# Kernel tuning notes

Hardware: AMD Instinct MI355X
Metric: run time of the kernel (lower is better)

## Reference

```python
import jax, jax.numpy as jnp
import numpy as np

EPS = 1e-5

def _ln(x, g, b):
    m = jnp.mean(x, axis=-1, keepdims=True)
    v = jnp.var(x, axis=-1, keepdims=True)
    return (x - m) / jnp.sqrt(v + EPS) * g + b

def _lin(x, w, b):
    # torch-style weight [out, in]
    return x @ w.T + b

def _mlp(x, w1, b1, w2, b2):
    # Mlp: Linear -> exact GELU -> Linear (dropout=0)
    return _lin(jax.nn.gelu(_lin(x, w1, b1), approximate=False), w2, b2)

def setup_inputs() -> dict:
    B, C, H, W = 2, 256, 64, 64
    key = jax.random.key(0)
    ks = jax.random.split(key, 32)
    s = 0.02  # param init scale keeps attention logits in a sane range
    d = {
        'center_fea': jax.random.normal(ks[0], (B, C, H, W), jnp.float32),
        'wh_fea':     jax.random.normal(ks[1], (B, C, H, W), jnp.float32),
        'cls_fea':    jax.random.normal(ks[2], (B, C, H, W), jnp.float32),
        'mix_w': jax.random.normal(ks[3], (C, 3 * C), jnp.float32) * s,
        'mix_b': jnp.zeros((C,), jnp.float32),
        'ln_g': jnp.ones((C,), jnp.float32),
        'ln_b': jnp.zeros((C,), jnp.float32),
        'q1_w': jax.random.normal(ks[4], (C, C), jnp.float32) * s,
        'q1_b': jnp.zeros((C,), jnp.float32),
        'q2_w': jax.random.normal(ks[5], (C, C), jnp.float32) * s,
        'q2_b': jnp.zeros((C,), jnp.float32),
        'q3_w': jax.random.normal(ks[6], (C, C), jnp.float32) * s,
        'q3_b': jnp.zeros((C,), jnp.float32),
        'k_w': jax.random.normal(ks[7], (C, C), jnp.float32) * s,
        'k_b': jnp.zeros((C,), jnp.float32),
        'v_w': jax.random.normal(ks[8], (C, C), jnp.float32) * s,
        'v_b': jnp.zeros((C,), jnp.float32),
        'cmlp_w1': jax.random.normal(ks[9], (C, C), jnp.float32) * s,
        'cmlp_b1': jnp.zeros((C,), jnp.float32),
        'cmlp_w2': jax.random.normal(ks[10], (C, C), jnp.float32) * s,
        'cmlp_b2': jnp.zeros((C,), jnp.float32),
        'wmlp_w1': jax.random.normal(ks[11], (C, C), jnp.float32) * s,
        'wmlp_b1': jnp.zeros((C,), jnp.float32),
        'wmlp_w2': jax.random.normal(ks[12], (C, C), jnp.float32) * s,
        'wmlp_b2': jnp.zeros((C,), jnp.float32),
        'clsmlp_w1': jax.random.normal(ks[13], (C, C), jnp.float32) * s,
        'clsmlp_b1': jnp.zeros((C,), jnp.float32),
        'clsmlp_w2': jax.random.normal(ks[14], (C, C), jnp.float32) * s,
        'clsmlp_b2': jnp.zeros((C,), jnp.float32),
    }
    return d

def reference(center_fea, wh_fea, cls_fea, mix_w, mix_b, ln_g, ln_b,
              q1_w, q1_b, q2_w, q2_b, q3_w, q3_b, k_w, k_b, v_w, v_b,
              cmlp_w1, cmlp_b1, cmlp_w2, cmlp_b2,
              wmlp_w1, wmlp_b1, wmlp_w2, wmlp_b2,
              clsmlp_w1, clsmlp_b1, clsmlp_w2, clsmlp_b2):
    b, c, h, w = center_fea.shape
    # 1x1 conv mix over concatenated channels [b, 3c, h, w] -> [b, c, h, w]
    cat = jnp.concatenate([center_fea, wh_fea, cls_fea], axis=1)
    mix = jnp.einsum('oc,bchw->bohw', mix_w, cat) + mix_b[None, :, None, None]

    tok = lambda x: x.reshape(b, c, h * w).transpose(0, 2, 1)  # [b, N, c]
    cf, wf, clf, mf = tok(center_fea), tok(wh_fea), tok(cls_fea), tok(mix)

    ct, wt, clt, mt = _ln(cf, ln_g, ln_b), _ln(wf, ln_g, ln_b), _ln(clf, ln_g, ln_b), _ln(mf, ln_g, ln_b)

    kf = _lin(mt, k_w, k_b)  # shared K
    vf = _lin(mt, v_w, v_b)  # shared V

    def attend(q):
        score = jax.nn.softmax(jnp.einsum('bnd,bmd->bnm', q, kf), axis=-1)  # [b, N, N]
        return jnp.einsum('bnm,bmd->bnd', score, vf)

    cf  = _ln(cf  + attend(_lin(ct,  q1_w, q1_b)), ln_g, ln_b)
    wf  = _ln(wf  + attend(_lin(wt,  q2_w, q2_b)), ln_g, ln_b)
    clf = _ln(clf + attend(_lin(clt, q3_w, q3_b)), ln_g, ln_b)

    cf  = _ln(cf  + _mlp(cf,  cmlp_w1, cmlp_b1, cmlp_w2, cmlp_b2), ln_g, ln_b)
    wf  = _ln(wf  + _mlp(wf,  wmlp_w1, wmlp_b1, wmlp_w2, wmlp_b2), ln_g, ln_b)
    clf = _ln(clf + _mlp(clf, clsmlp_w1, clsmlp_b1, clsmlp_w2, clsmlp_b2), ln_g, ln_b)

    untok = lambda x: x.transpose(0, 2, 1).reshape(b, c, h, w)
    return (untok(cf), untok(wf), untok(clf))
```

## Files before the change

kernel.cpp:

```cpp
#include <hip/hip_runtime.h>
#include <hip/hip_bf16.h>
#include <math.h>

typedef unsigned int   u32;
typedef unsigned short u16;
typedef float floatx4 __attribute__((ext_vector_type(4)));
typedef short bf16x8  __attribute__((ext_vector_type(8)));

#define MFMA16(a,b,c) __builtin_amdgcn_mfma_f32_16x16x32_bf16((a),(b),(c),0,0,0)

static __device__ __forceinline__ float bfbits2f(u16 h){
    return __uint_as_float(((u32)h) << 16);
}
static __device__ __forceinline__ u16 f2bfbits(float f){
    u32 u = __float_as_uint(f);
    u32 r = (u + 0x7fffu + ((u >> 16) & 1u)) >> 16;
    return (u16)r;
}
static __device__ __forceinline__ bool sniff_bf16(const void* ln_g){
    return ((const u32*)ln_g)[0] == 0x3f803f80u;
}

typedef __attribute__((address_space(1))) const unsigned int gas_u32;
typedef __attribute__((address_space(3))) unsigned int las_u32;
static __device__ __forceinline__ void gl_lds16(const void* g, void* l){
    __builtin_amdgcn_global_load_lds((gas_u32*)g, (las_u32*)l, 16, 0, 0);
}

#define DPPF(v, ctrl) __uint_as_float((u32)__builtin_amdgcn_update_dpp( \
        (int)__float_as_uint(v), (int)__float_as_uint(v), (ctrl), 0xf, 0xf, true))

static __device__ __forceinline__ float red16_max(float v){
    v = fmaxf(v, DPPF(v, 0xB1));
    v = fmaxf(v, DPPF(v, 0x4E));
    v = fmaxf(v, DPPF(v, 0x141));
    v = fmaxf(v, DPPF(v, 0x140));
    return v;
}
static __device__ __forceinline__ float red16_sum(float v){
    v += DPPF(v, 0xB1);
    v += DPPF(v, 0x4E);
    v += DPPF(v, 0x141);
    v += DPPF(v, 0x140);
    return v;
}

struct PackJob { const void* src; void* dst; int n; int mode; };
struct PackParams { PackJob jobs[26]; const void* lng; };

__global__ __launch_bounds__(256) void k_pack(PackParams p){
    bool isb = sniff_bf16(p.lng);
    PackJob j = p.jobs[blockIdx.y];
    for (int i = blockIdx.x * 256 + threadIdx.x; i < j.n; i += 256 * 256){
        float v = isb ? bfbits2f(((const u16*)j.src)[i]) : ((const float*)j.src)[i];
        if (j.mode == 0) ((u16*)j.dst)[i]  = f2bfbits(v);
        else             ((float*)j.dst)[i] = v;
    }
}

struct FtParams { const void* src[3]; u16* dst[3]; const void* lng; };

__global__ __launch_bounds__(256) void k_feat_t(FtParams p){
    bool isb = sniff_bf16(p.lng);
    int z = blockIdx.z; int si = z >> 1; int b = z & 1;
    const void* src = p.src[si]; u16* dst = p.dst[si];
    int n0 = blockIdx.x * 64, c0 = blockIdx.y * 64;
    __shared__ float tile[64][65];
    int t = threadIdx.x; int tx = t & 63; int ty = t >> 6;
    #pragma unroll
    for (int pp = 0; pp < 16; ++pp){
        int cl = ty + pp * 4;
        size_t off = ((size_t)b * 256 + c0 + cl) * 4096 + n0 + tx;
        float v = isb ? bfbits2f(((const u16*)src)[off]) : ((const float*)src)[off];
        tile[cl][tx] = v;
    }
    __syncthreads();
    #pragma unroll
    for (int pp = 0; pp < 16; ++pp){
        int nl = ty + pp * 4; int cl = tx;
        dst[((size_t)b * 4096 + n0 + nl) * 256 + c0 + cl] = f2bfbits(tile[cl][nl]);
    }
}

struct GemmJob { const u16* A0; const u16* A1; const u16* A2;
                 const u16* W; const float* bias; const u16* res; u16* out; };
struct GemmParams { GemmJob jobs[5]; int K; int op; };

__global__ __launch_bounds__(256, 3) void k_gemm(GemmParams p){
    GemmJob j = p.jobs[blockIdx.z];
    int m0 = blockIdx.x * 128, n0 = blockIdx.y * 128;
    __shared__ __align__(16) u16 As[128][64];
    __shared__ __align__(16) u16 Bs[128][64];
    int t = threadIdx.x;
    int wave = t >> 6, lane = t & 63, l15 = lane & 15, quad = lane >> 4;
    int mh = (wave & 1) * 64, nh = (wave >> 1) * 64;
    int key = l15 & 7;

    floatx4 acc[4][4];
    #pragma unroll
    for (int a = 0; a < 4; ++a)
        #pragma unroll
        for (int bq = 0; bq < 4; ++bq) acc[a][bq] = (floatx4){0.f,0.f,0.f,0.f};

    for (int k0 = 0; k0 < p.K; k0 += 64){
        __syncthreads();
        const u16* Ap = (k0 < 256) ? j.A0 : (k0 < 512 ? j.A1 : j.A2);
        int koff = k0 & 255;
        #pragma unroll
        for (int m = 0; m < 4; ++m){
            int r  = (wave * 4 + m) * 8 + (lane >> 3);
            int gs = (lane & 7) ^ (r & 7);
            gl_lds16(Ap  + (size_t)(m0 + r) * 256 + koff + gs * 8, &As[(wave*4+m)*8][0]);
            gl_lds16(j.W + (size_t)(n0 + r) * p.K + k0   + gs * 8, &Bs[(wave*4+m)*8][0]);
        }
        __syncthreads();

        #pragma unroll
        for (int kc = 0; kc < 2; ++kc){
            bf16x8 av[4], bv[4];
            #pragma unroll
            for (int mb = 0; mb < 4; ++mb)
                av[mb] = *(const bf16x8*)&As[mh + mb*16 + l15][(((kc*4 + quad) ^ key)) * 8];
            #pragma unroll
            for (int nb = 0; nb < 4; ++nb)
                bv[nb] = *(const bf16x8*)&Bs[nh + nb*16 + l15][(((kc*4 + quad) ^ key)) * 8];
            #pragma unroll
            for (int mb = 0; mb < 4; ++mb)
                #pragma unroll
                for (int nb = 0; nb < 4; ++nb)
                    acc[mb][nb] = MFMA16(av[mb], bv[nb], acc[mb][nb]);
        }
    }

    #pragma unroll
    for (int mb = 0; mb < 4; ++mb)
        #pragma unroll
        for (int nb = 0; nb < 4; ++nb){
            int col = n0 + nh + nb * 16 + l15;
            float bias = j.bias[col];
            #pragma unroll
            for (int rg = 0; rg < 4; ++rg){
                int row = m0 + mh + mb * 16 + quad * 4 + rg;
                float v = acc[mb][nb][rg] + bias;
                if (p.op == 1)      v = 0.5f * v * (1.0f + erff(v * 0.70710678118f));
                else if (p.op == 2) v += bfbits2f(j.res[(size_t)row * 256 + col]);
                j.out[(size_t)row * 256 + col] = f2bfbits(v);
            }
        }
}

struct LnJob { const u16* src; u16* dst; };
struct LnParams { LnJob jobs[4]; const float* g; const float* b; };

__global__ __launch_bounds__(256, 4) void k_ln(LnParams p){
    LnJob j = p.jobs[blockIdx.y];
    int g16 = threadIdx.x >> 4, l = threadIdx.x & 15;
    size_t tok = (size_t)blockIdx.x * 16 + g16;
    const u16* row = j.src + tok * 256 + l * 16;
    uint4 ra = *(const uint4*)(row);
    uint4 rb = *(const uint4*)(row + 8);
    u32 wv[8] = {ra.x, ra.y, ra.z, ra.w, rb.x, rb.y, rb.z, rb.w};
    float va[16];
    float s1 = 0.f, s2 = 0.f;
    #pragma unroll
    for (int i = 0; i < 8; ++i){
        float a = bfbits2f((u16)(wv[i] & 0xffffu));
        float c = bfbits2f((u16)(wv[i] >> 16));
        va[2*i] = a; va[2*i+1] = c;
        s1 += a + c; s2 += a*a + c*c;
    }
    s1 = red16_sum(s1); s2 = red16_sum(s2);
    float mean = s1 * (1.f/256.f);
    float var  = s2 * (1.f/256.f) - mean * mean;
    float rstd = rsqrtf(var + 1e-5f);
    int c0 = l * 16;
    u32 ow[8];
    #pragma unroll
    for (int i = 0; i < 8; ++i){
        float x0 = (va[2*i]   - mean) * rstd * p.g[c0 + 2*i]     + p.b[c0 + 2*i];
        float x1 = (va[2*i+1] - mean) * rstd * p.g[c0 + 2*i + 1] + p.b[c0 + 2*i + 1];
        ow[i] = (u32)f2bfbits(x0) | ((u32)f2bfbits(x1) << 16);
    }
    u16* dst = j.dst + tok * 256 + c0;
    *(uint4*)(dst)     = (uint4){ow[0], ow[1], ow[2], ow[3]};
    *(uint4*)(dst + 8) = (uint4){ow[4], ow[5], ow[6], ow[7]};
}

__global__ __launch_bounds__(256, 4) void k_vt(const u16* __restrict__ Vf, u16* __restrict__ Vt){
    int b = blockIdx.z;
    int n0 = blockIdx.x * 64, c0 = blockIdx.y * 64;
    __shared__ u16 tile[64][66];
    int t = threadIdx.x; int tx = t & 63; int ty = t >> 6;
    #pragma unroll
    for (int pp = 0; pp < 16; ++pp){
        int nl = ty + pp * 4;
        tile[nl][tx] = Vf[((size_t)b * 4096 + n0 + nl) * 256 + c0 + tx];
    }
    __syncthreads();
    #pragma unroll
    for (int pp = 0; pp < 16; ++pp){
        int cl = ty + pp * 4; int nl = tx;
        Vt[((size_t)b * 256 + c0 + cl) * 4096 + n0 + nl] = tile[nl][cl];
    }
}

struct FlashParams {
    const u16* Q[3]; const u16* K; const u16* Vt;
    const u16* Res[3]; u16* Out[3];
    const float* g; const float* b;
};

__global__ __launch_bounds__(256, 2) void k_flash(FlashParams p){
    int s = blockIdx.y >> 1, b = blockIdx.y & 1;
    int m0 = blockIdx.x * 64;
    const u16* Q   = p.Q[s]   + (size_t)b * 4096 * 256;
    const u16* Kf  = p.K      + (size_t)b * 4096 * 256;
    const u16* Vtg = p.Vt     + (size_t)b * 256 * 4096;
    const u16* Res = p.Res[s] + (size_t)b * 4096 * 256;
    u16*       Out = p.Out[s] + (size_t)b * 4096 * 256;

    __shared__ __align__(16) u16 Kb[2][32][256];
    __shared__ __align__(16) u16 Vb[2][256][32];
    __shared__ __align__(16) u16 Pl[4][16][40];

    int t = threadIdx.x, wave = t >> 6, lane = t & 63, l15 = lane & 15, quad = lane >> 4;

    auto stage = [&](int bi, int kv0){
        #pragma unroll
        for (int m = 0; m < 4; ++m){
            int q = wave * 4 + m;
            int r0 = q * 2 + (lane >> 5);
            int gg = (lane & 31) ^ (r0 & 7);
            gl_lds16(Kf + (size_t)(kv0 + r0) * 256 + gg * 8, &Kb[bi][q * 2][0]);
        }
        #pragma unroll
        for (int m = 0; m < 4; ++m){
            int q = wave * 4 + m;
            int d = q * 16 + (lane >> 2);
            int gg = (lane & 3) ^ ((d >> 1) & 3);
            gl_lds16(Vtg + (size_t)d * 4096 + kv0 + gg * 8, &Vb[bi][q * 16][0]);
        }
    };

    stage(0, 0);

    bf16x8 qf[8];
    {
        const u16* qrow = Q + (size_t)(m0 + wave * 16 + l15) * 256 + quad * 8;
        #pragma unroll
        for (int kc = 0; kc < 8; ++kc) qf[kc] = *(const bf16x8*)(qrow + kc * 32);
    }
    floatx4 o[16];
    #pragma unroll
    for (int i = 0; i < 16; ++i) o[i] = (floatx4){0.f,0.f,0.f,0.f};
    float mrow[4] = {-INFINITY,-INFINITY,-INFINITY,-INFINITY};
    float lsum[4] = {0.f,0.f,0.f,0.f};

    __syncthreads();
    int buf = 0;

    for (int ch = 0; ch < 128; ++ch){
        if (ch < 127) stage(buf ^ 1, (ch + 1) * 32);

        floatx4 sa[2];
        #pragma unroll
        for (int sub = 0; sub < 2; ++sub){
            int row = sub * 16 + l15;
            floatx4 a0 = (floatx4){0.f,0.f,0.f,0.f};
            floatx4 a1 = (floatx4){0.f,0.f,0.f,0.f};
            #pragma unroll
            for (int kc = 0; kc < 4; ++kc){
                bf16x8 kb0 = *(const bf16x8*)&Kb[buf][row][((((2*kc  ) * 4 + quad) ^ (row & 7))) * 8];
                bf16x8 kb1 = *(const bf16x8*)&Kb[buf][row][((((2*kc+1) * 4 + quad) ^ (row & 7))) * 8];
                a0 = MFMA16(qf[2*kc  ], kb0, a0);
                a1 = MFMA16(qf[2*kc+1], kb1, a1);
            }
            sa[sub] = a0 + a1;
        }

        float al[4]; int grow = 0;
        #pragma unroll
        for (int rg = 0; rg < 4; ++rg){
            float m1 = red16_max(fmaxf(sa[0][rg], sa[1][rg]));
            grow |= (m1 > mrow[rg]) ? 1 : 0;
            float mn = fmaxf(mrow[rg], m1);
            al[rg] = __expf(mrow[rg] - mn);
            mrow[rg] = mn;
        }
        #pragma unroll
        for (int rg = 0; rg < 4; ++rg){
            float p0 = __expf(sa[0][rg] - mrow[rg]);
            float p1 = __expf(sa[1][rg] - mrow[rg]);
            sa[0][rg] = p0; sa[1][rg] = p1;
            lsum[rg] = lsum[rg] * al[rg] + (p0 + p1);
        }

        #pragma unroll
        for (int sub = 0; sub < 2; ++sub)
            #pragma unroll
            for (int rg = 0; rg < 4; ++rg)
                Pl[wave][quad * 4 + rg][sub * 16 + l15] = f2bfbits(sa[sub][rg]);

        if (__any(grow)){
            #pragma unroll
            for (int dc = 0; dc < 16; ++dc)
                #pragma unroll
                for (int rg = 0; rg < 4; ++rg) o[dc][rg] *= al[rg];
        }

        asm volatile("s_waitcnt lgkmcnt(0)" ::: "memory");
        __builtin_amdgcn_sched_barrier(0);

        bf16x8 pa = *(const bf16x8*)&Pl[wave][l15][quad * 8];
        #pragma unroll
        for (int dc = 0; dc < 16; ++dc){
            int row = dc * 16 + l15;
            bf16x8 vb = *(const bf16x8*)&Vb[buf][row][((quad ^ ((row >> 1) & 3))) * 8];
            o[dc] = MFMA16(pa, vb, o[dc]);
        }

        __syncthreads();
        buf ^= 1;
    }

    float inv[4];
    #pragma unroll
    for (int rg = 0; rg < 4; ++rg) inv[rg] = 1.0f / red16_sum(lsum[rg]);
    float s1[4] = {0.f,0.f,0.f,0.f}, s2[4] = {0.f,0.f,0.f,0.f};
    #pragma unroll
    for (int dc = 0; dc < 16; ++dc)
        #pragma unroll
        for (int rg = 0; rg < 4; ++rg){
            int row = m0 + wave * 16 + quad * 4 + rg;
            float v = o[dc][rg] * inv[rg] + bfbits2f(Res[(size_t)row * 256 + dc * 16 + l15]);
            o[dc][rg] = v;
            s1[rg] += v; s2[rg] += v * v;
        }
    #pragma unroll
    for (int rg = 0; rg < 4; ++rg){
        float mean = red16_sum(s1[rg]) * (1.f/256.f);
        float q2   = red16_sum(s2[rg]);
        float var  = q2 * (1.f/256.f) - mean * mean;
        s1[rg] = mean; s2[rg] = rsqrtf(var + 1e-5f);
    }
    #pragma unroll
    for (int dc = 0; dc < 16; ++dc){
        int c = dc * 16 + l15;
        float gv = p.g[c], bv = p.b[c];
        #pragma unroll
        for (int rg = 0; rg < 4; ++rg){
            int row = m0 + wave * 16 + quad * 4 + rg;
            Out[(size_t)row * 256 + c] = f2bfbits((o[dc][rg] - s1[rg]) * s2[rg] * gv + bv);
        }
    }
}

struct OutTParams { const u16* F[3]; void* out; const void* lng; };

__global__ __launch_bounds__(256, 4) void k_out_t(OutTParams p){
    bool isb = sniff_bf16(p.lng);
    int z = blockIdx.z; int s = z >> 1; int b = z & 1;
    const u16* F = p.F[s];
    int n0 = blockIdx.x * 64, c0 = blockIdx.y * 64;
    __shared__ u16 tile[64][66];
    int t = threadIdx.x; int tx = t & 63; int ty = t >> 6;
    #pragma unroll
    for (int pp = 0; pp < 16; ++pp){
        int nl = ty + pp * 4;
        tile[nl][tx] = F[((size_t)b * 4096 + n0 + nl) * 256 + c0 + tx];
    }
    __syncthreads();
    size_t obase = ((size_t)s * 2 + b) * 256 * 4096;
    #pragma unroll
    for (int pp = 0; pp < 16; ++pp){
        int cl = ty + pp * 4; int nl = tx;
        u16 raw = tile[nl][cl];
        size_t off = obase + (size_t)(c0 + cl) * 4096 + n0 + nl;
        if (isb) ((u16*)p.out)[off]   = raw;
        else     ((float*)p.out)[off] = bfbits2f(raw);
    }
}

extern "C" void kernel_launch(void* const* d_in, const int* in_sizes, int n_in,
                              void* d_out, int out_size, void* d_ws, size_t ws_size,
                              hipStream_t stream) {
    (void)in_sizes; (void)n_in; (void)out_size; (void)ws_size;
    const size_t SLOT = (size_t)2 * 4096 * 256;
    u16* ws = (u16*)d_ws;
    auto slot = [&](int i){ return ws + (size_t)i * SLOT; };

    u16 *Tc = slot(0),  *Tw = slot(1),  *Tcl = slot(2),  *Tm = slot(3);
    u16 *Lc = slot(4),  *Lw = slot(5),  *Lcl = slot(6),  *Lm = slot(7);
    u16 *Q1 = slot(8),  *Q2 = slot(9),  *Q3  = slot(10);
    u16 *Kf = slot(11), *Vf = slot(12), *Vt  = slot(13);
    u16 *Yc = slot(14), *Yw = slot(15), *Ycl = slot(16);
    u16 *Hc = Q1, *Hw = Q2, *Hcl = Q3;
    u16 *Zc = Lc, *Zw = Lw, *Zcl = Lcl;
    u16 *Fc = Kf, *Fw = Vf, *Fcl = Vt;

    u16* wbase = slot(17);
    u16 *mixw = wbase;
    u16 *q1w = wbase + 196608, *q2w = q1w + 65536, *q3w = q2w + 65536;
    u16 *kw  = q3w + 65536,    *vw  = kw  + 65536;
    u16 *cw1 = vw  + 65536, *cw2 = cw1 + 65536, *ww1 = cw2 + 65536,
        *ww2 = ww1 + 65536, *clw1 = ww2 + 65536, *clw2 = clw1 + 65536;
    float* pbase = (float*)(wbase + 1048576);
    float *mixb = pbase,        *lng = pbase+256,  *lnb = pbase+512,
          *q1b = pbase+768,  *q2b = pbase+1024, *q3b = pbase+1280,
          *kb  = pbase+1536, *vb  = pbase+1792,
          *cb1 = pbase+2048, *cb2 = pbase+2304, *wb1 = pbase+2560,
          *wb2 = pbase+2816, *clb1= pbase+3072, *clb2= pbase+3328;

    {
        PackParams pp;
        const int widx[12] = {3,7,9,11,13,15,17,19,21,23,25,27};
        u16* wdst[12] = {mixw,q1w,q2w,q3w,kw,vw,cw1,cw2,ww1,ww2,clw1,clw2};
        for (int i = 0; i < 12; ++i)
            pp.jobs[i] = PackJob{ d_in[widx[i]], wdst[i], (i==0?196608:65536), 0 };
        const int pidx[14] = {4,5,6,8,10,12,14,16,18,20,22,24,26,28};
        float* pdst[14] = {mixb,lng,lnb,q1b,q2b,q3b,kb,vb,cb1,cb2,wb1,wb2,clb1,clb2};
        for (int i = 0; i < 14; ++i)
            pp.jobs[12+i] = PackJob{ d_in[pidx[i]], pdst[i], 256, 1 };
        pp.lng = d_in[5];
        hipLaunchKernelGGL(k_pack, dim3(256, 26), dim3(256), 0, stream, pp);
    }
    {
        FtParams fp;
        fp.src[0] = d_in[0]; fp.src[1] = d_in[1]; fp.src[2] = d_in[2];
        fp.dst[0] = Tc; fp.dst[1] = Tw; fp.dst[2] = Tcl;
        fp.lng = d_in[5];
        hipLaunchKernelGGL(k_feat_t, dim3(64, 4, 6), dim3(256), 0, stream, fp);
    }
    {
        GemmParams gp; gp.K = 768; gp.op = 0;
        gp.jobs[0] = GemmJob{ Tc, Tw, Tcl, mixw, mixb, nullptr, Tm };
        hipLaunchKernelGGL(k_gemm, dim3(64, 2, 1), dim3(256), 0, stream, gp);
    }
    {
        LnParams lp; lp.g = lng; lp.b = lnb;
        lp.jobs[0] = LnJob{Tc, Lc}; lp.jobs[1] = LnJob{Tw, Lw};
        lp.jobs[2] = LnJob{Tcl, Lcl}; lp.jobs[3] = LnJob{Tm, Lm};
        hipLaunchKernelGGL(k_ln, dim3(512, 4), dim3(256), 0, stream, lp);
    }
    {
        GemmParams gp; gp.K = 256; gp.op = 0;
        gp.jobs[0] = GemmJob{ Lc,  nullptr, nullptr, q1w, q1b, nullptr, Q1 };
        gp.jobs[1] = GemmJob{ Lw,  nullptr, nullptr, q2w, q2b, nullptr, Q2 };
        gp.jobs[2] = GemmJob{ Lcl, nullptr, nullptr, q3w, q3b, nullptr, Q3 };
        gp.jobs[3] = GemmJob{ Lm,  nullptr, nullptr, kw,  kb,  nullptr, Kf };
        gp.jobs[4] = GemmJob{ Lm,  nullptr, nullptr, vw,  vb,  nullptr, Vf };
        hipLaunchKernelGGL(k_gemm, dim3(64, 2, 5), dim3(256), 0, stream, gp);
    }
    hipLaunchKernelGGL(k_vt, dim3(64, 4, 2), dim3(256), 0, stream, Vf, Vt);
    {
        FlashParams fp;
        fp.Q[0] = Q1; fp.Q[1] = Q2; fp.Q[2] = Q3;
        fp.K = Kf; fp.Vt = Vt;
        fp.Res[0] = Tc; fp.Res[1] = Tw; fp.Res[2] = Tcl;
        fp.Out[0] = Yc; fp.Out[1] = Yw; fp.Out[2] = Ycl;
        fp.g = lng; fp.b = lnb;
        hipLaunchKernelGGL(k_flash, dim3(64, 6), dim3(256), 0, stream, fp);
    }
    {
        GemmParams gp; gp.K = 256; gp.op = 1;
        gp.jobs[0] = GemmJob{ Yc,  nullptr, nullptr, cw1,  cb1,  nullptr, Hc };
        gp.jobs[1] = GemmJob{ Yw,  nullptr, nullptr, ww1,  wb1,  nullptr, Hw };
        gp.jobs[2] = GemmJob{ Ycl, nullptr, nullptr, clw1, clb1, nullptr, Hcl };
        hipLaunchKernelGGL(k_gemm, dim3(64, 2, 3), dim3(256), 0, stream, gp);
    }
    {
        GemmParams gp; gp.K = 256; gp.op = 2;
        gp.jobs[0] = GemmJob{ Hc,  nullptr, nullptr, cw2,  cb2,  Yc,  Zc };
        gp.jobs[1] = GemmJob{ Hw,  nullptr, nullptr, ww2,  wb2,  Yw,  Zw };
        gp.jobs[2] = GemmJob{ Hcl, nullptr, nullptr, clw2, clb2, Ycl, Zcl };
        hipLaunchKernelGGL(k_gemm, dim3(64, 2, 3), dim3(256), 0, stream, gp);
    }
    {
        LnParams lp; lp.g = lng; lp.b = lnb;
        lp.jobs[0] = LnJob{Zc, Fc}; lp.jobs[1] = LnJob{Zw, Fw};
        lp.jobs[2] = LnJob{Zcl, Fcl}; lp.jobs[3] = LnJob{Zc, Fc};
        hipLaunchKernelGGL(k_ln, dim3(512, 3), dim3(256), 0, stream, lp);
    }
    {
        OutTParams op;
        op.F[0] = Fc; op.F[1] = Fw; op.F[2] = Fcl;
        op.out = d_out; op.lng = d_in[5];
        hipLaunchKernelGGL(k_out_t, dim3(64, 4, 6), dim3(256), 0, stream, op);
    }
}
```

Before: 468.1 us.

## Shrink GEMM tiles to 64x64 with double-buffered LDS and raise flash MFMA priority

The shared GEMM kernel moves from 128x128 to 64x64 output tiles, with double-buffered LDS staging so the next K-slice loads while the current one is computed. The grid grows fourfold so more of the CUs are busy on these small GEMMs. The flash attention kernel wraps its MFMA sections in s_setprio to favor matrix issue across waves. Smaller tiles reduce per-block data reuse and add more global traffic.

```diff
diff --git a/kernel.cpp b/kernel.cpp
--- a/kernel.cpp
+++ b/kernel.cpp
@@ -86,56 +86,61 @@
                  const u16* W; const float* bias; const u16* res; u16* out; };
 struct GemmParams { GemmJob jobs[5]; int K; int op; };
 
-__global__ __launch_bounds__(256, 3) void k_gemm(GemmParams p){
+__global__ __launch_bounds__(256, 4) void k_gemm(GemmParams p){
     GemmJob j = p.jobs[blockIdx.z];
-    int m0 = blockIdx.x * 128, n0 = blockIdx.y * 128;
-    __shared__ __align__(16) u16 As[128][64];
-    __shared__ __align__(16) u16 Bs[128][64];
+    int m0 = blockIdx.x * 64, n0 = blockIdx.y * 64;
+    __shared__ __align__(16) u16 As[2][64][64];
+    __shared__ __align__(16) u16 Bs[2][64][64];
     int t = threadIdx.x;
     int wave = t >> 6, lane = t & 63, l15 = lane & 15, quad = lane >> 4;
-    int mh = (wave & 1) * 64, nh = (wave >> 1) * 64;
+    int mh = (wave & 1) * 32, nh = (wave >> 1) * 32;
     int key = l15 & 7;
 
-    floatx4 acc[4][4];
-    #pragma unroll
-    for (int a = 0; a < 4; ++a)
-        #pragma unroll
-        for (int bq = 0; bq < 4; ++bq) acc[a][bq] = (floatx4){0.f,0.f,0.f,0.f};
-
-    for (int k0 = 0; k0 < p.K; k0 += 64){
-        __syncthreads();
+    auto stage = [&](int bi, int k0){
         const u16* Ap = (k0 < 256) ? j.A0 : (k0 < 512 ? j.A1 : j.A2);
         int koff = k0 & 255;
         #pragma unroll
-        for (int m = 0; m < 4; ++m){
-            int r  = (wave * 4 + m) * 8 + (lane >> 3);
+        for (int i = 0; i < 2; ++i){
+            int rq = wave * 2 + i;
+            int r  = rq * 8 + (lane >> 3);
             int gs = (lane & 7) ^ (r & 7);
-            gl_lds16(Ap  + (size_t)(m0 + r) * 256 + koff + gs * 8, &As[(wave*4+m)*8][0]);
-            gl_lds16(j.W + (size_t)(n0 + r) * p.K + k0   + gs * 8, &Bs[(wave*4+m)*8][0]);
+            gl_lds16(Ap  + (size_t)(m0 + r) * 256 + koff + gs * 8, &As[bi][rq * 8][0]);
+            gl_lds16(j.W + (size_t)(n0 + r) * p.K + k0   + gs * 8, &Bs[bi][rq * 8][0]);
+        }
+    };
+
+    floatx4 acc[2][2];
+    #pragma unroll
+    for (int a = 0; a < 2; ++a)
+        #pragma unroll
+        for (int bq = 0; bq < 2; ++bq) acc[a][bq] = (floatx4){0.f,0.f,0.f,0.f};
+
+    stage(0, 0);
+    __syncthreads();
+    int nk = p.K >> 6, buf = 0;
+
+    for (int ks = 0; ks < nk; ++ks){
+        if (ks + 1 < nk) stage(buf ^ 1, (ks + 1) * 64);
+        #pragma unroll
+        for (int kc = 0; kc < 2; ++kc){
+            int gsel = ((kc * 4 + quad) ^ key) * 8;
+            bf16x8 a0 = *(const bf16x8*)&As[buf][mh +      l15][gsel];
+            bf16x8 a1 = *(const bf16x8*)&As[buf][mh + 16 + l15][gsel];
+            bf16x8 b0 = *(const bf16x8*)&Bs[buf][nh +      l15][gsel];
+            bf16x8 b1 = *(const bf16x8*)&Bs[buf][nh + 16 + l15][gsel];
+            acc[0][0] = MFMA16(a0, b0, acc[0][0]);
+            acc[0][1] = MFMA16(a0, b1, acc[0][1]);
+            acc[1][0] = MFMA16(a1, b0, acc[1][0]);
+            acc[1][1] = MFMA16(a1, b1, acc[1][1]);
         }
         __syncthreads();
-
-        #pragma unroll
-        for (int kc = 0; kc < 2; ++kc){
-            bf16x8 av[4], bv[4];
-            #pragma unroll
-            for (int mb = 0; mb < 4; ++mb)
-                av[mb] = *(const bf16x8*)&As[mh + mb*16 + l15][(((kc*4 + quad) ^ key)) * 8];
-            #pragma unroll
-            for (int nb = 0; nb < 4; ++nb)
-                bv[nb] = *(const bf16x8*)&Bs[nh + nb*16 + l15][(((kc*4 + quad) ^ key)) * 8];
-            #pragma unroll
-            for (int mb = 0; mb < 4; ++mb)
-                #pragma unroll
-                for (int nb = 0; nb < 4; ++nb)
-                    acc[mb][nb] = MFMA16(av[mb], bv[nb], acc[mb][nb]);
-        }
-    }
-
-    #pragma unroll
-    for (int mb = 0; mb < 4; ++mb)
-        #pragma unroll
-        for (int nb = 0; nb < 4; ++nb){
+        buf ^= 1;
+    }
+
+    #pragma unroll
+    for (int mb = 0; mb < 2; ++mb)
+        #pragma unroll
+        for (int nb = 0; nb < 2; ++nb){
             int col = n0 + nh + nb * 16 + l15;
             float bias = j.bias[col];
             #pragma unroll
@@ -263,6 +268,7 @@
         if (ch < 127) stage(buf ^ 1, (ch + 1) * 32);
 
         floatx4 sa[2];
+        __builtin_amdgcn_s_setprio(1);
         #pragma unroll
         for (int sub = 0; sub < 2; ++sub){
             int row = sub * 16 + l15;
@@ -277,6 +283,7 @@
             }
             sa[sub] = a0 + a1;
         }
+        __builtin_amdgcn_s_setprio(0);
 
         float al[4]; int grow = 0;
         #pragma unroll
@@ -312,12 +319,14 @@
         __builtin_amdgcn_sched_barrier(0);
 
         bf16x8 pa = *(const bf16x8*)&Pl[wave][l15][quad * 8];
+        __builtin_amdgcn_s_setprio(1);
         #pragma unroll
         for (int dc = 0; dc < 16; ++dc){
             int row = dc * 16 + l15;
             bf16x8 vb = *(const bf16x8*)&Vb[buf][row][((quad ^ ((row >> 1) & 3))) * 8];
             o[dc] = MFMA16(pa, vb, o[dc]);
         }
+        __builtin_amdgcn_s_setprio(0);
 
         __syncthreads();
         buf ^= 1;
@@ -434,7 +443,7 @@
     {
         GemmParams gp; gp.K = 768; gp.op = 0;
         gp.jobs[0] = GemmJob{ Tc, Tw, Tcl, mixw, mixb, nullptr, Tm };
-        hipLaunchKernelGGL(k_gemm, dim3(64, 2, 1), dim3(256), 0, stream, gp);
+        hipLaunchKernelGGL(k_gemm, dim3(128, 4, 1), dim3(256), 0, stream, gp);
     }
     {
         LnParams lp; lp.g = lng; lp.b = lnb;
@@ -449,7 +458,7 @@
         gp.jobs[2] = GemmJob{ Lcl, nullptr, nullptr, q3w, q3b, nullptr, Q3 };
         gp.jobs[3] = GemmJob{ Lm,  nullptr, nullptr, kw,  kb,  nullptr, Kf };
         gp.jobs[4] = GemmJob{ Lm,  nullptr, nullptr, vw,  vb,  nullptr, Vf };
-        hipLaunchKernelGGL(k_gemm, dim3(64, 2, 5), dim3(256), 0, stream, gp);
+        hipLaunchKernelGGL(k_gemm, dim3(128, 4, 5), dim3(256), 0, stream, gp);
     }
     hipLaunchKernelGGL(k_vt, dim3(64, 4, 2), dim3(256), 0, stream, Vf, Vt);
     {
@@ -466,14 +475,14 @@
         gp.jobs[0] = GemmJob{ Yc,  nullptr, nullptr, cw1,  cb1,  nullptr, Hc };
         gp.jobs[1] = GemmJob{ Yw,  nullptr, nullptr, ww1,  wb1,  nullptr, Hw };
         gp.jobs[2] = GemmJob{ Ycl, nullptr, nullptr, clw1, clb1, nullptr, Hcl };
-        hipLaunchKernelGGL(k_gemm, dim3(64, 2, 3), dim3(256), 0, stream, gp);
+        hipLaunchKernelGGL(k_gemm, dim3(128, 4, 3), dim3(256), 0, stream, gp);
     }
     {
         GemmParams gp; gp.K = 256; gp.op = 2;
         gp.jobs[0] = GemmJob{ Hc,  nullptr, nullptr, cw2,  cb2,  Yc,  Zc };
         gp.jobs[1] = GemmJob{ Hw,  nullptr, nullptr, ww2,  wb2,  Yw,  Zw };
         gp.jobs[2] = GemmJob{ Hcl, nullptr, nullptr, clw2, clb2, Ycl, Zcl };
-        hipLaunchKernelGGL(k_gemm, dim3(64, 2, 3), dim3(256), 0, stream, gp);
+        hipLaunchKernelGGL(k_gemm, dim3(128, 4, 3), dim3(256), 0, stream, gp);
     }
     {
         LnParams lp; lp.g = lng; lp.b = lnb;
```

New measurement: 426.2 us. 1.1x faster.
